# Optimization experiments

Hardware: AMD Instinct MI355X
Metric: run time of the kernel (lower is better)

Reference implementation:

```python
import jax, jax.numpy as jnp
import numpy as np

LMAX = 4  # number of l blocks (lmax+1 in the original)
# segment ids mapping the L2 = sum(2l+1) = 16 spherical components to their l block
SEG = np.repeat(np.arange(LMAX), 2 * np.arange(LMAX) + 1)  # [16]
SEG_ONEHOT = np.eye(LMAX, dtype=np.float32)[SEG]  # [16, LMAX]


def setup_inputs() -> dict:
    key = jax.random.key(0)
    ks = jax.random.split(key, 10)
    b, m, f, k, L2 = 16, 64, 128, 64, 16
    def rnd(kk, shape, scale):
        return jax.random.normal(kk, shape, dtype=jnp.float32) * scale
    return {
        'x': rnd(ks[0], (b, m, f, L2), 1.0),
        'y': rnd(ks[1], (b, m, f, L2), 1.0),
        'wx0': rnd(ks[2], (k, f, f, LMAX), 1.0 / np.sqrt(f * f * LMAX)),
        'wy0': rnd(ks[3], (k, f, f, LMAX), 1.0 / np.sqrt(f * f * LMAX)),
        'wx_mlp': rnd(ks[4], (2, k, k), 1.0 / np.sqrt(k)),
        'bx_mlp': rnd(ks[5], (2, k, k), 0.02),
        'wy_mlp': rnd(ks[6], (2, k, k), 1.0 / np.sqrt(k)),
        'by_mlp': rnd(ks[7], (2, k, k), 0.02),
        'wxf': rnd(ks[8], (LMAX, f, k), 1.0 / np.sqrt(k)),
        'wyf': rnd(ks[9], (LMAX, f, k), 1.0 / np.sqrt(k)),
    }


def reference(x, y, wx0, wy0, wx_mlp, bx_mlp, wy_mlp, by_mlp, wxf, wyf):
    act = jax.nn.silu
    S = jnp.asarray(SEG_ONEHOT)  # [L2, lmax]
    # outer product of y and x features, segment-summed over each l block:
    # mix[b,m,fy,fx,l] = sum_c y[b,m,fy,c] * x[b,m,fx,c] * S[c,l]
    mix = jnp.einsum('bmfc,bmgc,cl->bmfgl', y, x, S)  # [b,m,f,f,lmax]
    mx = jnp.einsum('bmfgl,kfgl->bmk', mix, wx0)
    my = jnp.einsum('bmfgl,kfgl->bmk', mix, wy0)
    for i in range(wx_mlp.shape[0]):  # the n_mlp-1 used MLP stages
        mx = act(jnp.einsum('bmk,kl->bml', mx, wx_mlp[i]) + bx_mlp[i])
        my = act(jnp.einsum('bmk,kl->bml', my, wy_mlp[i]) + by_mlp[i])
    mx = act(jnp.einsum('bmk,lfk->bmfl', mx, wxf))  # [b,m,f,lmax]
    my = act(jnp.einsum('bmk,lfk->bmfl', my, wyf))
    # broadcast each l gate over its 2l+1 components (repeat == gather by SEG)
    seg = jnp.asarray(SEG)
    res = mx[..., seg] * x + my[..., seg] * y  # [b,m,f,L2]
    return res
```

## Files before the change

kernel.cpp:

```cpp
#include <hip/hip_runtime.h>
#include <stdint.h>


#define AS1 __attribute__((address_space(1)))
#define AS3 __attribute__((address_space(3)))

typedef __bf16 bf16x8 __attribute__((ext_vector_type(8)));
typedef float f32x4 __attribute__((ext_vector_type(4)));

__device__ __forceinline__ uint16_t f2b(float f) {
  uint32_t u = __float_as_uint(f);
  u += 0x7fffu + ((u >> 16) & 1u);
  return (uint16_t)(u >> 16);
}

#if __has_builtin(__builtin_amdgcn_fdot2_f32_bf16)
typedef __bf16 bf16x2 __attribute__((ext_vector_type(2)));
__device__ __forceinline__ float dot2b(uint32_t a, uint32_t b, float c) {
  union { uint32_t u; bf16x2 v; } ua, ub;
  ua.u = a; ub.u = b;
  return __builtin_amdgcn_fdot2_f32_bf16(ua.v, ub.v, c, false);
}
#else
__device__ __forceinline__ float dot2b(uint32_t a, uint32_t b, float c) {
  float a0 = __uint_as_float(a << 16), a1 = __uint_as_float(a & 0xffff0000u);
  float b0 = __uint_as_float(b << 16), b1 = __uint_as_float(b & 0xffff0000u);
  return c + a0 * b0 + a1 * b1;
}
#endif

__global__ __launch_bounds__(256) void convert_all(
    const float* __restrict__ wx0, const float* __restrict__ wy0,
    const float* __restrict__ x, const float* __restrict__ y,
    const float* __restrict__ wxf, const float* __restrict__ wyf,
    uint16_t* __restrict__ Wb, uint16_t* __restrict__ xb,
    uint16_t* __restrict__ yb, float* __restrict__ wfT) {
  if (blockIdx.x >= 6144) {
    int base = (blockIdx.x - 6144) * 2048 + threadIdx.x * 8;
#pragma unroll
    for (int ii = 0; ii < 8; ++ii) {
      int idx = base + ii;
      int side = idx >> 15, rem = idx & 32767;
      int k = rem >> 9, l = (rem >> 7) & 3, f = rem & 127;
      const float* src = side ? wyf : wxf;
      wfT[idx] = src[((size_t)l * 128 + f) * 64 + k];
    }
    return;
  }
  size_t i = ((size_t)blockIdx.x * 256 + threadIdx.x) * 8;
  const float* s; uint16_t* d;
  if (i < 4194304)        { s = wx0 + i;              d = Wb + i; }
  else if (i < 8388608)   { s = wy0 + (i - 4194304);  d = Wb + i; }
  else if (i < 10485760)  { s = x + (i - 8388608);    d = xb + (i - 8388608); }
  else                    { s = y + (i - 10485760);   d = yb + (i - 10485760); }
  float4 v0 = *(const float4*)s;
  float4 v1 = *(const float4*)(s + 4);
  uint32_t o0 = (uint32_t)f2b(v0.x) | ((uint32_t)f2b(v0.y) << 16);
  uint32_t o1 = (uint32_t)f2b(v0.z) | ((uint32_t)f2b(v0.w) << 16);
  uint32_t o2 = (uint32_t)f2b(v1.x) | ((uint32_t)f2b(v1.y) << 16);
  uint32_t o3 = (uint32_t)f2b(v1.z) | ((uint32_t)f2b(v1.w) << 16);
  *(uint4*)d = make_uint4(o0, o1, o2, o3);
}

__device__ __forceinline__ void gload_lds16(const void* g, void* l) {
  __builtin_amdgcn_global_load_lds((const AS1 uint32_t*)g, (AS3 uint32_t*)l, 16, 0, 0);
}

#define PIPE_BAR(N) \
  asm volatile("s_waitcnt vmcnt(" #N ") lgkmcnt(0)\n\ts_barrier" ::: "memory")

__global__ __launch_bounds__(256, 2) void fused_gemm(
    const uint16_t* __restrict__ xb, const uint16_t* __restrict__ yb,
    const uint16_t* __restrict__ Wb, float* __restrict__ Cpart) {
  __shared__ __align__(16) uint16_t sA[2][128 * 40];
  __shared__ __align__(16) uint16_t sB[3][128 * 32];
  __shared__ __align__(16) uint16_t yS[3][2048];

  int tid = threadIdx.x;
  int w = tid >> 6, lane = tid & 63;
  int g_id = blockIdx.x;
  int fb = g_id >> 2, fyg = g_id & 3;
  int FB = fb * 8;
  int fy0 = fyg * 32;
  int m0 = blockIdx.y * 128;
  int r = lane & 15, q = lane >> 4;
  int wm = w >> 1, wn = w & 1;
  int rowl = lane >> 2, qq = lane & 3;
  int m_loc = tid & 127, half = tid >> 7;

  uint32_t xr[32];
  {
    const uint16_t* xp0 = xb + (size_t)(m0 + m_loc) * 2048 + (FB + half * 4) * 16;
#pragma unroll
    for (int j = 0; j < 8; ++j) {
      uint4 v = *(const uint4*)(xp0 + j * 8);
      xr[j * 4 + 0] = v.x; xr[j * 4 + 1] = v.y;
      xr[j * 4 + 2] = v.z; xr[j * 4 + 3] = v.w;
    }
  }

  f32x4 zero = {0.f, 0.f, 0.f, 0.f};
  f32x4 acc[4][4];
#pragma unroll
  for (int i = 0; i < 4; ++i)
#pragma unroll
    for (int j = 0; j < 4; ++j) acc[i][j] = zero;

  int bcol = qq ^ ((rowl >> 1) & 3);
  int ychunk = w >> 1, ymbase = (w & 1) * 64;
  const uint16_t* ysrc_base = yb + (size_t)(m0 + ymbase + lane) * 2048 + ychunk * 8;
  int ydst_off = ychunk * 1024 + ymbase * 8;

  auto issueB = [&](uint16_t* dstB, int t) {
    int kk0 = (fy0 + t) * 512 + FB * 4;
#pragma unroll
    for (int jj = 0; jj < 2; ++jj) {
      int blk = w * 2 + jj;
      int rowi = blk * 16 + rowl;
      gload_lds16(Wb + (size_t)rowi * 65536 + kk0 + bcol * 8, dstB + blk * 512);
    }
  };
  auto issueY = [&](uint16_t* dstY, int t) {
    gload_lds16(ysrc_base + (size_t)(fy0 + t) * 16, dstY + ydst_off);
  };
  auto computeG = [&](const uint16_t* srcY, float* gg) {
    uint4 ya = *(const uint4*)(srcY + m_loc * 8);
    uint4 yc = *(const uint4*)(srcY + 1024 + m_loc * 8);
    uint32_t yp[8] = {ya.x, ya.y, ya.z, ya.w, yc.x, yc.y, yc.z, yc.w};
    uint32_t yl0 = yp[0] & 0xffffu, yh0 = yp[0] & 0xffff0000u;
    uint32_t yl4 = yp[4] & 0xffffu, yh4 = yp[4] & 0xffff0000u;
#pragma unroll
    for (int fxp = 0; fxp < 4; ++fxp) {
      const uint32_t* xp = xr + fxp * 8;
      gg[fxp * 4 + 0] = dot2b(xp[0], yl0, 0.f);
      gg[fxp * 4 + 1] = dot2b(xp[1], yp[1], dot2b(xp[0], yh0, 0.f));
      gg[fxp * 4 + 2] = dot2b(xp[4], yl4,
                         dot2b(xp[3], yp[3], dot2b(xp[2], yp[2], 0.f)));
      gg[fxp * 4 + 3] = dot2b(xp[7], yp[7], dot2b(xp[6], yp[6],
                         dot2b(xp[5], yp[5], dot2b(xp[4], yh4, 0.f))));
    }
  };
  auto writeA = [&](uint16_t* dstA, const float* gg) {
    uint32_t o[8];
#pragma unroll
    for (int p = 0; p < 8; ++p)
      o[p] = (__float_as_uint(gg[2 * p]) >> 16) |
             (__float_as_uint(gg[2 * p + 1]) & 0xffff0000u);
    uint16_t* dst = dstA + m_loc * 40 + half * 16;
    *(uint4*)dst       = make_uint4(o[0], o[1], o[2], o[3]);
    *(uint4*)(dst + 8) = make_uint4(o[4], o[5], o[6], o[7]);
  };

  float gg[16];
  issueY(yS[0], 0);
  __syncthreads();
  computeG(yS[0], gg);
  writeA(sA[0], gg);
  issueB(sB[0], 0);
  issueY(yS[1], 1);
  issueB(sB[1], 1);
  issueY(yS[2], 2);
  PIPE_BAR(3);

  uint16_t *pAc = sA[0], *pAn = sA[1];
  uint16_t *pBread = sB[0], *pBmid = sB[1], *pBissue = sB[2];
  uint16_t *pYcomp = yS[1], *pYmid = yS[2], *pYissue = yS[0];

  for (int t = 0; t < 32; ++t) {
    if (t <= 29) issueB(pBissue, t + 2);
    if (t <= 28) issueY(pYissue, t + 3);

    bf16x8 a[4], b[4];
#pragma unroll
    for (int i = 0; i < 4; ++i)
      a[i] = *(const bf16x8*)&pAc[(wm * 64 + i * 16 + r) * 40 + q * 8];
#pragma unroll
    for (int j = 0; j < 4; ++j) {
      int row = wn * 64 + j * 16 + r;
      int pos = q ^ ((row >> 1) & 3);
      b[j] = *(const bf16x8*)&pBread[row * 32 + pos * 8];
    }

    if (t < 31) {
      computeG(pYcomp, gg);
      writeA(pAn, gg);
    }

    __builtin_amdgcn_s_setprio(1);
#pragma unroll
    for (int i = 0; i < 4; ++i)
#pragma unroll
      for (int j = 0; j < 4; ++j)
        acc[i][j] = __builtin_amdgcn_mfma_f32_16x16x32_bf16(a[i], b[j], acc[i][j], 0, 0, 0);
    __builtin_amdgcn_s_setprio(0);

    if (t <= 28)      PIPE_BAR(3);
    else if (t == 29) PIPE_BAR(2);
    else if (t == 30) PIPE_BAR(0);

    uint16_t* tp;
    tp = pAc; pAc = pAn; pAn = tp;
    tp = pBread; pBread = pBmid; pBmid = pBissue; pBissue = tp;
    tp = pYcomp; pYcomp = pYmid; pYmid = pYissue; pYissue = tp;
  }

  float* cbase = Cpart + (size_t)g_id * 131072;
#pragma unroll
  for (int i = 0; i < 4; ++i)
#pragma unroll
    for (int j = 0; j < 4; ++j)
#pragma unroll
      for (int reg = 0; reg < 4; ++reg) {
        int mm = m0 + wm * 64 + i * 16 + q * 4 + reg;
        int nn = wn * 64 + j * 16 + r;
        cbase[(size_t)mm * 128 + nn] = acc[i][j][reg];
      }
}

__global__ __launch_bounds__(256) void finish_kernel(
    const float* __restrict__ x, const float* __restrict__ y,
    const float* __restrict__ wx_mlp, const float* __restrict__ bx_mlp,
    const float* __restrict__ wy_mlp, const float* __restrict__ by_mlp,
    const float* __restrict__ wfT,
    const float* __restrict__ Cpart, float* __restrict__ out) {
  const int seg[16] = {0,1,1,1,2,2,2,2,2,3,3,3,3,3,3,3};
  __shared__ float sred[256];
  __shared__ float sm[128];
  __shared__ float sg[2][128][4];
  int t = threadIdx.x;
  int bm = blockIdx.x;
  int mi = bm & 63;

  {
    int col = t & 127, hh = t >> 7;
    const float* cp = Cpart + (size_t)(hh * 32) * 131072 + (size_t)bm * 128 + col;
    float s = 0.f;
#pragma unroll 8
    for (int sp = 0; sp < 32; ++sp)
      s += cp[(size_t)sp * 131072];
    sred[t] = s;
  }
  __syncthreads();
  if (t < 128) sm[t] = sred[t] + sred[t + 128];
  __syncthreads();

  for (int st = 0; st < 2; ++st) {
    float v = 0.f;
    if (t < 128) {
      int side = t >> 6, j = t & 63;
      const float* wmlp = side ? wy_mlp : wx_mlp;
      const float* bmlp = side ? by_mlp : bx_mlp;
      const float* mv = sm + side * 64;
#pragma unroll 8
      for (int k = 0; k < 64; ++k)
        v += mv[k] * wmlp[(st * 64 + k) * 64 + j];
      v += bmlp[(st * 64 + mi) * 64 + j];
      v = v / (1.f + __expf(-v));
    }
    __syncthreads();
    if (t < 128) sm[t] = v;
    __syncthreads();
  }

  {
    int side = t >> 7, f = t & 127;
    const float* base = wfT + side * 32768;
    const float* mv = sm + side * 64;
    float gg[4] = {0.f, 0.f, 0.f, 0.f};
#pragma unroll 8
    for (int k = 0; k < 64; ++k) {
      float m2 = mv[k];
#pragma unroll
      for (int l = 0; l < 4; ++l)
        gg[l] += m2 * base[(k * 4 + l) * 128 + f];
    }
#pragma unroll
    for (int l = 0; l < 4; ++l)
      sg[side][f][l] = gg[l] / (1.f + __expf(-gg[l]));
  }
  __syncthreads();

  {
    int f = t >> 1, half = t & 1;
    size_t base = ((size_t)bm * 128 + f) * 16 + half * 8;
    float4 xa = *(const float4*)(x + base), xb4 = *(const float4*)(x + base + 4);
    float4 ya = *(const float4*)(y + base), yb4 = *(const float4*)(y + base + 4);
    float xv[8] = {xa.x, xa.y, xa.z, xa.w, xb4.x, xb4.y, xb4.z, xb4.w};
    float yv[8] = {ya.x, ya.y, ya.z, ya.w, yb4.x, yb4.y, yb4.z, yb4.w};
    float o[8];
#pragma unroll
    for (int ii = 0; ii < 8; ++ii) {
      int c = half * 8 + ii;
      o[ii] = sg[0][f][seg[c]] * xv[ii] + sg[1][f][seg[c]] * yv[ii];
    }
    *(float4*)(out + base)     = make_float4(o[0], o[1], o[2], o[3]);
    *(float4*)(out + base + 4) = make_float4(o[4], o[5], o[6], o[7]);
  }
}

extern "C" void kernel_launch(void* const* d_in, const int* in_sizes, int n_in,
                              void* d_out, int out_size, void* d_ws, size_t ws_size,
                              hipStream_t stream) {
  const float* x      = (const float*)d_in[0];
  const float* y      = (const float*)d_in[1];
  const float* wx0    = (const float*)d_in[2];
  const float* wy0    = (const float*)d_in[3];
  const float* wx_mlp = (const float*)d_in[4];
  const float* bx_mlp = (const float*)d_in[5];
  const float* wy_mlp = (const float*)d_in[6];
  const float* by_mlp = (const float*)d_in[7];
  const float* wxf    = (const float*)d_in[8];
  const float* wyf    = (const float*)d_in[9];
  float* out = (float*)d_out;

  uint16_t* Wb    = (uint16_t*)d_ws;
  uint16_t* xb    = (uint16_t*)((char*)d_ws + (size_t)16777216);
  uint16_t* yb    = (uint16_t*)((char*)d_ws + (size_t)20971520);
  float*    Cpart = (float*)((char*)d_ws + (size_t)25165824);
  float*    wfT   = (float*)((char*)d_ws + (size_t)58720256);

  convert_all<<<6176, 256, 0, stream>>>(wx0, wy0, x, y, wxf, wyf, Wb, xb, yb, wfT);
  fused_gemm<<<dim3(64, 8), 256, 0, stream>>>(xb, yb, Wb, Cpart);
  finish_kernel<<<1024, 256, 0, stream>>>(x, y, wx_mlp, bx_mlp, wy_mlp, by_mlp,
                                          wfT, Cpart, out);
}
```

Before: 169.4 us.

## Pre-tile weights into swizzled blocks and widen GEMM block to 512 threads

The conversion kernel now writes the bf16 weights in a pre-tiled, swizzled layout, so each GEMM K-step's B tile is one contiguous 8 KB chunk loaded with coalesced 16-byte LDS-direct loads. The GEMM block grows to 8 waves. Four waves load the B tile and four load the y tile, with per-group waitcnt depths, and each wave computes a 64x32 output tile. The A tile now uses an XOR-swizzled 32-wide layout instead of 40-wide padding, which cuts LDS size. The intent is better global-load coalescing, more waves per CU for latency hiding, and less work per thread in the y·x product, at the cost of more barrier participants and more duplicated A-fragment reads.

```diff
diff --git a/kernel.cpp b/kernel.cpp
--- a/kernel.cpp
+++ b/kernel.cpp
@@ -33,10 +33,31 @@
     const float* __restrict__ wx0, const float* __restrict__ wy0,
     const float* __restrict__ x, const float* __restrict__ y,
     const float* __restrict__ wxf, const float* __restrict__ wyf,
-    uint16_t* __restrict__ Wb, uint16_t* __restrict__ xb,
+    uint16_t* __restrict__ Wb2, uint16_t* __restrict__ xb,
     uint16_t* __restrict__ yb, float* __restrict__ wfT) {
-  if (blockIdx.x >= 6144) {
-    int base = (blockIdx.x - 6144) * 2048 + threadIdx.x * 8;
+  int bid = blockIdx.x, tid = threadIdx.x;
+  if (bid < 4096) {
+    int c = bid * 256 + tid;
+    int fb = c >> 16;
+    int rem = c & 65535;
+    int fy = rem >> 9;
+    int rem2 = rem & 511;
+    int n = rem2 >> 2, pos = rem2 & 3;
+    int slot = pos ^ ((n >> 1) & 3);
+    int k = n & 63;
+    const float* src = (n < 64 ? wx0 : wy0) +
+        ((size_t)(k * 128 + fy) * 512 + fb * 32 + slot * 8);
+    float4 v0 = *(const float4*)src;
+    float4 v1 = *(const float4*)(src + 4);
+    uint32_t o0 = (uint32_t)f2b(v0.x) | ((uint32_t)f2b(v0.y) << 16);
+    uint32_t o1 = (uint32_t)f2b(v0.z) | ((uint32_t)f2b(v0.w) << 16);
+    uint32_t o2 = (uint32_t)f2b(v1.x) | ((uint32_t)f2b(v1.y) << 16);
+    uint32_t o3 = (uint32_t)f2b(v1.z) | ((uint32_t)f2b(v1.w) << 16);
+    *(uint4*)(Wb2 + (size_t)c * 8) = make_uint4(o0, o1, o2, o3);
+    return;
+  }
+  if (bid >= 6144) {
+    int base = (bid - 6144) * 2048 + tid * 8;
 #pragma unroll
     for (int ii = 0; ii < 8; ++ii) {
       int idx = base + ii;
@@ -47,12 +68,10 @@
     }
     return;
   }
-  size_t i = ((size_t)blockIdx.x * 256 + threadIdx.x) * 8;
+  size_t i = ((size_t)(bid - 4096) * 256 + tid) * 8;
   const float* s; uint16_t* d;
-  if (i < 4194304)        { s = wx0 + i;              d = Wb + i; }
-  else if (i < 8388608)   { s = wy0 + (i - 4194304);  d = Wb + i; }
-  else if (i < 10485760)  { s = x + (i - 8388608);    d = xb + (i - 8388608); }
-  else                    { s = y + (i - 10485760);   d = yb + (i - 10485760); }
+  if (i < 2097152) { s = x + i;             d = xb + i; }
+  else             { s = y + (i - 2097152); d = yb + (i - 2097152); }
   float4 v0 = *(const float4*)s;
   float4 v1 = *(const float4*)(s + 4);
   uint32_t o0 = (uint32_t)f2b(v0.x) | ((uint32_t)f2b(v0.y) << 16);
@@ -69,10 +88,10 @@
 #define PIPE_BAR(N) \
   asm volatile("s_waitcnt vmcnt(" #N ") lgkmcnt(0)\n\ts_barrier" ::: "memory")
 
-__global__ __launch_bounds__(256, 2) void fused_gemm(
+__global__ __launch_bounds__(512, 4) void fused_gemm(
     const uint16_t* __restrict__ xb, const uint16_t* __restrict__ yb,
-    const uint16_t* __restrict__ Wb, float* __restrict__ Cpart) {
-  __shared__ __align__(16) uint16_t sA[2][128 * 40];
+    const uint16_t* __restrict__ Wb2, float* __restrict__ Cpart) {
+  __shared__ __align__(16) uint16_t sA[2][128 * 32];
   __shared__ __align__(16) uint16_t sB[3][128 * 32];
   __shared__ __align__(16) uint16_t yS[3][2048];
 
@@ -84,15 +103,14 @@
   int fy0 = fyg * 32;
   int m0 = blockIdx.y * 128;
   int r = lane & 15, q = lane >> 4;
-  int wm = w >> 1, wn = w & 1;
-  int rowl = lane >> 2, qq = lane & 3;
-  int m_loc = tid & 127, half = tid >> 7;
-
-  uint32_t xr[32];
+  int wm = w >> 2, wn = w & 3;
+  int m_loc = tid & 127, quarter = tid >> 7;
+
+  uint32_t xr[16];
   {
-    const uint16_t* xp0 = xb + (size_t)(m0 + m_loc) * 2048 + (FB + half * 4) * 16;
-#pragma unroll
-    for (int j = 0; j < 8; ++j) {
+    const uint16_t* xp0 = xb + (size_t)(m0 + m_loc) * 2048 + (FB + quarter * 2) * 16;
+#pragma unroll
+    for (int j = 0; j < 4; ++j) {
       uint4 v = *(const uint4*)(xp0 + j * 8);
       xr[j * 4 + 0] = v.x; xr[j * 4 + 1] = v.y;
       xr[j * 4 + 2] = v.z; xr[j * 4 + 3] = v.w;
@@ -100,29 +118,29 @@
   }
 
   f32x4 zero = {0.f, 0.f, 0.f, 0.f};
-  f32x4 acc[4][4];
+  f32x4 acc[4][2];
 #pragma unroll
   for (int i = 0; i < 4; ++i)
 #pragma unroll
-    for (int j = 0; j < 4; ++j) acc[i][j] = zero;
-
-  int bcol = qq ^ ((rowl >> 1) & 3);
-  int ychunk = w >> 1, ymbase = (w & 1) * 64;
+    for (int j = 0; j < 2; ++j) acc[i][j] = zero;
+
+  auto issueB = [&](uint16_t* dstB, int t) {
+    if (w < 4) {
+      size_t base = (size_t)(fb * 128 + fy0 + t) * 4096;
+#pragma unroll
+      for (int jj = 0; jj < 2; ++jj) {
+        int blk = w * 2 + jj;
+        gload_lds16(Wb2 + base + blk * 512 + lane * 8, dstB + blk * 512);
+      }
+    }
+  };
+  int ychunk = (w >> 1) & 1, ymbase = (w & 1) * 64;
   const uint16_t* ysrc_base = yb + (size_t)(m0 + ymbase + lane) * 2048 + ychunk * 8;
   int ydst_off = ychunk * 1024 + ymbase * 8;
-
-  auto issueB = [&](uint16_t* dstB, int t) {
-    int kk0 = (fy0 + t) * 512 + FB * 4;
-#pragma unroll
-    for (int jj = 0; jj < 2; ++jj) {
-      int blk = w * 2 + jj;
-      int rowi = blk * 16 + rowl;
-      gload_lds16(Wb + (size_t)rowi * 65536 + kk0 + bcol * 8, dstB + blk * 512);
-    }
+  auto issueY = [&](uint16_t* dstY, int t) {
+    if (w >= 4) gload_lds16(ysrc_base + (size_t)(fy0 + t) * 16, dstY + ydst_off);
   };
-  auto issueY = [&](uint16_t* dstY, int t) {
-    gload_lds16(ysrc_base + (size_t)(fy0 + t) * 16, dstY + ydst_off);
-  };
+
   auto computeG = [&](const uint16_t* srcY, float* gg) {
     uint4 ya = *(const uint4*)(srcY + m_loc * 8);
     uint4 yc = *(const uint4*)(srcY + 1024 + m_loc * 8);
@@ -130,7 +148,7 @@
     uint32_t yl0 = yp[0] & 0xffffu, yh0 = yp[0] & 0xffff0000u;
     uint32_t yl4 = yp[4] & 0xffffu, yh4 = yp[4] & 0xffff0000u;
 #pragma unroll
-    for (int fxp = 0; fxp < 4; ++fxp) {
+    for (int fxp = 0; fxp < 2; ++fxp) {
       const uint32_t* xp = xr + fxp * 8;
       gg[fxp * 4 + 0] = dot2b(xp[0], yl0, 0.f);
       gg[fxp * 4 + 1] = dot2b(xp[1], yp[1], dot2b(xp[0], yh0, 0.f));
@@ -141,17 +159,16 @@
     }
   };
   auto writeA = [&](uint16_t* dstA, const float* gg) {
-    uint32_t o[8];
-#pragma unroll
-    for (int p = 0; p < 8; ++p)
+    uint32_t o[4];
+#pragma unroll
+    for (int p = 0; p < 4; ++p)
       o[p] = (__float_as_uint(gg[2 * p]) >> 16) |
              (__float_as_uint(gg[2 * p + 1]) & 0xffff0000u);
-    uint16_t* dst = dstA + m_loc * 40 + half * 16;
-    *(uint4*)dst       = make_uint4(o[0], o[1], o[2], o[3]);
-    *(uint4*)(dst + 8) = make_uint4(o[4], o[5], o[6], o[7]);
+    int pos = quarter ^ ((m_loc >> 1) & 3);
+    *(uint4*)(dstA + m_loc * 32 + pos * 8) = make_uint4(o[0], o[1], o[2], o[3]);
   };
 
-  float gg[16];
+  float gg[8];
   issueY(yS[0], 0);
   __syncthreads();
   computeG(yS[0], gg);
@@ -160,7 +177,7 @@
   issueY(yS[1], 1);
   issueB(sB[1], 1);
   issueY(yS[2], 2);
-  PIPE_BAR(3);
+  if (w < 4) PIPE_BAR(2); else PIPE_BAR(1);
 
   uint16_t *pAc = sA[0], *pAn = sA[1];
   uint16_t *pBread = sB[0], *pBmid = sB[1], *pBissue = sB[2];
@@ -170,13 +187,16 @@
     if (t <= 29) issueB(pBissue, t + 2);
     if (t <= 28) issueY(pYissue, t + 3);
 
-    bf16x8 a[4], b[4];
-#pragma unroll
-    for (int i = 0; i < 4; ++i)
-      a[i] = *(const bf16x8*)&pAc[(wm * 64 + i * 16 + r) * 40 + q * 8];
-#pragma unroll
-    for (int j = 0; j < 4; ++j) {
-      int row = wn * 64 + j * 16 + r;
+    bf16x8 a[4], b[2];
+#pragma unroll
+    for (int i = 0; i < 4; ++i) {
+      int row = wm * 64 + i * 16 + r;
+      int pos = q ^ ((row >> 1) & 3);
+      a[i] = *(const bf16x8*)&pAc[row * 32 + pos * 8];
+    }
+#pragma unroll
+    for (int j = 0; j < 2; ++j) {
+      int row = wn * 32 + j * 16 + r;
       int pos = q ^ ((row >> 1) & 3);
       b[j] = *(const bf16x8*)&pBread[row * 32 + pos * 8];
     }
@@ -190,12 +210,12 @@
 #pragma unroll
     for (int i = 0; i < 4; ++i)
 #pragma unroll
-      for (int j = 0; j < 4; ++j)
+      for (int j = 0; j < 2; ++j)
         acc[i][j] = __builtin_amdgcn_mfma_f32_16x16x32_bf16(a[i], b[j], acc[i][j], 0, 0, 0);
     __builtin_amdgcn_s_setprio(0);
 
-    if (t <= 28)      PIPE_BAR(3);
-    else if (t == 29) PIPE_BAR(2);
+    if (t <= 28)      { if (w < 4) PIPE_BAR(2); else PIPE_BAR(1); }
+    else if (t == 29) { if (w < 4) PIPE_BAR(2); else PIPE_BAR(0); }
     else if (t == 30) PIPE_BAR(0);
 
     uint16_t* tp;
@@ -208,11 +228,11 @@
 #pragma unroll
   for (int i = 0; i < 4; ++i)
 #pragma unroll
-    for (int j = 0; j < 4; ++j)
+    for (int j = 0; j < 2; ++j)
 #pragma unroll
       for (int reg = 0; reg < 4; ++reg) {
         int mm = m0 + wm * 64 + i * 16 + q * 4 + reg;
-        int nn = wn * 64 + j * 16 + r;
+        int nn = wn * 32 + j * 16 + r;
         cbase[(size_t)mm * 128 + nn] = acc[i][j][reg];
       }
 }
@@ -313,14 +333,14 @@
   const float* wyf    = (const float*)d_in[9];
   float* out = (float*)d_out;
 
-  uint16_t* Wb    = (uint16_t*)d_ws;
+  uint16_t* Wb2   = (uint16_t*)d_ws;
   uint16_t* xb    = (uint16_t*)((char*)d_ws + (size_t)16777216);
   uint16_t* yb    = (uint16_t*)((char*)d_ws + (size_t)20971520);
   float*    Cpart = (float*)((char*)d_ws + (size_t)25165824);
   float*    wfT   = (float*)((char*)d_ws + (size_t)58720256);
 
-  convert_all<<<6176, 256, 0, stream>>>(wx0, wy0, x, y, wxf, wyf, Wb, xb, yb, wfT);
-  fused_gemm<<<dim3(64, 8), 256, 0, stream>>>(xb, yb, Wb, Cpart);
+  convert_all<<<6176, 256, 0, stream>>>(wx0, wy0, x, y, wxf, wyf, Wb2, xb, yb, wfT);
+  fused_gemm<<<dim3(64, 8), 512, 0, stream>>>(xb, yb, Wb2, Cpart);
   finish_kernel<<<1024, 256, 0, stream>>>(x, y, wx_mlp, bx_mlp, wy_mlp, by_mlp,
                                           wfT, Cpart, out);
 }
```

After: 166.1 us. -2.0%, faster.
